# Performance work log

Measured on AMD Instinct MI355X. Metric: run time of the kernel, lower is better.

Reference implementation:

```python
import jax, jax.numpy as jnp
import numpy as np

NUM_HEADS = 16
ROPE_BASE = 10000.0


def _rope_tables(head_dim, seq_len, dtype=jnp.float32):
    # Half-split convention: rotate first half against second half.
    inv_freq = 1.0 / (ROPE_BASE ** (jnp.arange(0, head_dim, 2, dtype=dtype) / head_dim))
    pos = jnp.arange(seq_len, dtype=dtype)
    angles_half = jnp.einsum('s,d->sd', pos, inv_freq)          # (S, D/2)
    angles = jnp.concatenate([angles_half, angles_half], -1)     # (S, D)
    return jnp.cos(angles), jnp.sin(angles)


def _apply_rope(x, cos, sin):
    # x: (H, S, D); cos/sin: (S, D) broadcast over heads
    half = x.shape[-1] // 2
    x1, x2 = x[..., :half], x[..., half:]
    x_rot = jnp.concatenate([-x2, x1], axis=-1)
    return x * cos + x_rot * sin


def setup_inputs() -> dict:
    key = jax.random.key(0)
    S, E = 2048, 2048
    ks = jax.random.split(key, 9)
    sc = 0.02
    return {
        'x': jax.random.normal(ks[0], (S, E), jnp.float32),
        'Wq': jax.random.normal(ks[1], (E, E), jnp.float32) * sc,
        'bq': jax.random.normal(ks[2], (E,), jnp.float32) * sc,
        'Wk': jax.random.normal(ks[3], (E, E), jnp.float32) * sc,
        'bk': jax.random.normal(ks[4], (E,), jnp.float32) * sc,
        'Wv': jax.random.normal(ks[5], (E, E), jnp.float32) * sc,
        'bv': jax.random.normal(ks[6], (E,), jnp.float32) * sc,
        'Wo': jax.random.normal(ks[7], (E, E), jnp.float32) * sc,
        'bo': jax.random.normal(ks[8], (E,), jnp.float32) * sc,
    }


def reference(x, Wq, bq, Wk, bk, Wv, bv, Wo, bo):
    S, E = x.shape
    H = NUM_HEADS
    D = E // H
    scale = D ** 0.5
    cos, sin = _rope_tables(D, S, x.dtype)

    def proj(W, b):
        return (x @ W.T + b).reshape(S, H, D).transpose(1, 0, 2)  # (H, S, D)

    q = _apply_rope(proj(Wq, bq), cos, sin)
    k = _apply_rope(proj(Wk, bk), cos, sin)
    v = proj(Wv, bv)

    scores = jnp.einsum('hsd,htd->hst', q, k) / scale  # (H, S, S)
    attn = jax.nn.softmax(scores, axis=-1)
    out = jnp.einsum('hst,htd->hsd', attn, v)          # (H, S, D)
    # Faithful to the original's transpose(0,1).view(S,E) on a (1,H,S,D)
    # tensor: an in-order (head-major) flatten reinterpreted as (S, E).
    out = out.reshape(S, E)
    return out @ Wo.T + bo
```

## Files before the change

kernel.cpp:

```cpp
#include <hip/hip_runtime.h>

#define SDIM 2048
#define EDIM 2048
#define NHEAD 16
#define DHEAD 128

typedef __attribute__((ext_vector_type(8))) short short8;
typedef __attribute__((ext_vector_type(4))) float floatx4;

__device__ __forceinline__ float bf2f(ushort u) {
    union { uint i; float f; } v; v.i = ((uint)u) << 16; return v.f;
}
__device__ __forceinline__ ushort f2bf(float f) {
    union { float f; uint i; } v; v.f = f;
    uint r = v.i + 0x7fff + ((v.i >> 16) & 1);
    return (ushort)(r >> 16);
}

__device__ __forceinline__ void gload_lds16(const ushort* g, ushort* l) {
    __builtin_amdgcn_global_load_lds(
        (const __attribute__((address_space(1))) void*)g,
        (__attribute__((address_space(3))) void*)l, 16, 0, 0);
}

__global__ void convert5_kernel(
    const float* __restrict__ s0, const float* __restrict__ s1,
    const float* __restrict__ s2, const float* __restrict__ s3,
    const float* __restrict__ s4,
    ushort* __restrict__ d0, ushort* __restrict__ d1,
    ushort* __restrict__ d2, ushort* __restrict__ d3,
    ushort* __restrict__ d4)
{
    const float* src; ushort* dst;
    switch (blockIdx.y) {
        case 0: src = s0; dst = d0; break;
        case 1: src = s1; dst = d1; break;
        case 2: src = s2; dst = d2; break;
        case 3: src = s3; dst = d3; break;
        default: src = s4; dst = d4; break;
    }
    int i = blockIdx.x * blockDim.x + threadIdx.x;
    float4 f = ((const float4*)src)[i];
    ushort4 o;
    o.x = f2bf(f.x); o.y = f2bf(f.y); o.z = f2bf(f.z); o.w = f2bf(f.w);
    ((ushort4*)dst)[i] = o;
}

#define QPRESCALE 0.12754245f
__global__ void rope_kernel(ushort* __restrict__ Q, ushort* __restrict__ K) {
    int t = blockIdx.x * blockDim.x + threadIdx.x;
    int arr = t >> 18;
    int r = t & 0x3FFFF;
    int g = r & 7;
    int h = (r >> 3) & 15;
    int s = r >> 7;
    ushort* P = arr ? K : Q;
    float qsc = arr ? 1.0f : QPRESCALE;
    size_t base = ((size_t)s << 11) + (h << 7) + g * 8;
    union { uint4 v; ushort u[8]; } x1, x2, o1, o2;
    x1.v = *(const uint4*)(P + base);
    x2.v = *(const uint4*)(P + base + 64);
    float fs = (float)s;
#pragma unroll
    for (int j = 0; j < 8; j++) {
        int i = g * 8 + j;
        float inv = __expf((float)i * -0.14391157f);
        float ang = fs * inv;
        float rev = ang * 0.15915494309f;
        rev = rev - floorf(rev);
        float ar = rev * 6.28318530718f;
        float sn = __sinf(ar), cs = __cosf(ar);
        float a = bf2f(x1.u[j]), b = bf2f(x2.u[j]);
        o1.u[j] = f2bf((a * cs - b * sn) * qsc);
        o2.u[j] = f2bf((b * cs + a * sn) * qsc);
    }
    *(uint4*)(P + base) = o1.v;
    *(uint4*)(P + base + 64) = o2.v;
}

__device__ __forceinline__ void stout(float* p, float v)  { *p = v; }
__device__ __forceinline__ void stout(ushort* p, float v) { *p = f2bf(v); }

template <typename OUTT>
__global__ __launch_bounds__(256) void gemm_bt(
    const ushort* __restrict__ A,
    const ushort* __restrict__ B0, const ushort* __restrict__ B1, const ushort* __restrict__ B2,
    const float* __restrict__ s0, const float* __restrict__ s1, const float* __restrict__ s2,
    OUTT* __restrict__ C0, OUTT* __restrict__ C1, OUTT* __restrict__ C2,
    int nbpm, int vt_which)
{
    __shared__ __align__(16) ushort a_s[128 * 32];
    __shared__ __align__(16) ushort b_s[128 * 32];

    const int tid = threadIdx.x;
    const int wave = tid >> 6, lane = tid & 63;
    const int l15 = lane & 15, quad = lane >> 4;
    const int wm = wave & 1, wn = wave >> 1;

    const int w = blockIdx.x;
    const int xcd = w & 7, t = w >> 3;
    const int Y = gridDim.x >> 4;
    const int mtile = ((xcd & 1) << 3) | (t & 7);
    const int y = (Y >> 2) * (xcd >> 1) + (t >> 3);
    const int bm = mtile * 128;
    const int which = y / nbpm;
    const int n0 = (y % nbpm) * 128;

    const ushort* B   = (which == 0) ? B0 : (which == 1) ? B1 : B2;
    const float*  bia = (which == 0) ? s0 : (which == 1) ? s1 : s2;
    OUTT*         C   = (which == 0) ? C0 : (which == 1) ? C1 : C2;

    floatx4 acc[4][4];
#pragma unroll
    for (int i = 0; i < 4; i++)
#pragma unroll
        for (int j = 0; j < 4; j++) acc[i][j] = (floatx4)0.0f;

    const int t1 = tid + 256;
    const int row0 = tid >> 2, kc0 = (tid & 3) * 8;
    const int row1 = t1 >> 2,  kc1 = (t1 & 3) * 8;

    for (int k0 = 0; k0 < EDIM; k0 += 32) {
        __syncthreads();
        gload_lds16(A + (size_t)(bm + row0) * EDIM + k0 + kc0, a_s + tid * 8);
        gload_lds16(A + (size_t)(bm + row1) * EDIM + k0 + kc1, a_s + t1 * 8);
        gload_lds16(B + (size_t)(n0 + row0) * EDIM + k0 + kc0, b_s + tid * 8);
        gload_lds16(B + (size_t)(n0 + row1) * EDIM + k0 + kc1, b_s + t1 * 8);
        __syncthreads();

        short8 af[4], bf[4];
#pragma unroll
        for (int mt = 0; mt < 4; mt++)
            af[mt] = *(const short8*)(a_s + (wm * 64 + mt * 16 + l15) * 32 + quad * 8);
#pragma unroll
        for (int nt = 0; nt < 4; nt++)
            bf[nt] = *(const short8*)(b_s + (wn * 64 + nt * 16 + l15) * 32 + quad * 8);
#pragma unroll
        for (int mt = 0; mt < 4; mt++)
#pragma unroll
            for (int nt = 0; nt < 4; nt++)
                acc[mt][nt] = __builtin_amdgcn_mfma_f32_16x16x32_bf16(af[mt], bf[nt], acc[mt][nt], 0, 0, 0);
    }

    if (which == vt_which) {
        ushort* Cv = (ushort*)C;
#pragma unroll
        for (int nt = 0; nt < 4; nt++) {
            int col = n0 + wn * 64 + nt * 16 + l15;
            int h = col >> 7, d = col & 127;
            float bv = bia[col];
#pragma unroll
            for (int mt = 0; mt < 4; mt++) {
                int s = bm + wm * 64 + mt * 16 + quad * 4;
                ushort4 pk;
                pk.x = f2bf(acc[mt][nt][0] + bv);
                pk.y = f2bf(acc[mt][nt][1] + bv);
                pk.z = f2bf(acc[mt][nt][2] + bv);
                pk.w = f2bf(acc[mt][nt][3] + bv);
                *(ushort4*)(Cv + (size_t)h * SDIM * DHEAD + (size_t)d * SDIM + s) = pk;
            }
        }
    } else {
#pragma unroll
        for (int nt = 0; nt < 4; nt++) {
            int col = n0 + wn * 64 + nt * 16 + l15;
            float bv = bia[col];
#pragma unroll
            for (int mt = 0; mt < 4; mt++) {
#pragma unroll
                for (int r = 0; r < 4; r++) {
                    int row = bm + wm * 64 + mt * 16 + quad * 4 + r;
                    stout(&C[(size_t)row * EDIM + col], acc[mt][nt][r] + bv);
                }
            }
        }
    }
}

#define MFIX2 17.31234049f
__global__ __launch_bounds__(256, 4) void attn_kernel(
    const ushort* __restrict__ Q, const ushort* __restrict__ K,
    const ushort* __restrict__ Vtg,
    ushort* __restrict__ Opart, float* __restrict__ Lsum,
    ushort* __restrict__ Ab, int nsplit)
{
    __shared__ __align__(16) ushort Ks[64 * 128];
    __shared__ __align__(16) ushort Vt[128 * 64];
    __shared__ __align__(16) ushort Ps[64 * 64];

    const int bid = blockIdx.x;
    const int head = bid & 15, qt = (bid >> 4) & 31, half = bid >> 9;
    const int tid = threadIdx.x, wave = tid >> 6, lane = tid & 63;
    const int l15 = lane & 15, quad = lane >> 4;
    const int l7 = l15 & 7;
    const int kstart = half * (SDIM / nsplit);
    const int ntile = (SDIM / nsplit) / 64;

    short8 qf[4];
    {
        int s = qt * 64 + wave * 16 + l15;
        const ushort* qp = Q + (size_t)s * EDIM + head * DHEAD;
#pragma unroll
        for (int kc = 0; kc < 4; kc++) qf[kc] = *(const short8*)(qp + kc * 32 + quad * 8);
    }

    floatx4 o[8];
#pragma unroll
    for (int i = 0; i < 8; i++) o[i] = (floatx4)0.0f;
    float lsum = 0.0f;

    const int krow = tid >> 4, kc8 = tid & 15;
    const int vd = tid >> 3, vc8 = tid & 7;
    const int prow = wave * 16 + l15;

    for (int kv = 0; kv < ntile; kv++) {
        const int k0 = kstart + kv * 64;
        __syncthreads();
#pragma unroll
        for (int i = 0; i < 4; i++) {
            int row = krow + i * 16;
            uint4 v = *(const uint4*)(K + (size_t)(k0 + row) * EDIM + head * DHEAD + kc8 * 8);
            *(uint4*)(Ks + row * 128 + ((kc8 ^ (row & 7)) << 3)) = v;
        }
#pragma unroll
        for (int i = 0; i < 4; i++) {
            int d = vd + i * 32;
            uint4 v = *(const uint4*)(Vtg + (size_t)head * SDIM * DHEAD + (size_t)d * SDIM + k0 + vc8 * 8);
            *(uint4*)(Vt + d * 64 + ((vc8 ^ (d & 7)) << 3)) = v;
        }
        __syncthreads();

#pragma unroll
        for (int nt = 0; nt < 4; nt++) {
            floatx4 st = (floatx4)0.0f;
#pragma unroll
            for (int kc = 0; kc < 4; kc++) {
                short8 kfr = *(const short8*)(Ks + (nt * 16 + l15) * 128 + (((kc * 4 + quad) ^ l7) << 3));
                st = __builtin_amdgcn_mfma_f32_16x16x32_bf16(kfr, qf[kc], st, 0, 0, 0);
            }
            ushort4 pk;
            float p0 = __builtin_amdgcn_exp2f(st[0] - MFIX2);
            float p1 = __builtin_amdgcn_exp2f(st[1] - MFIX2);
            float p2 = __builtin_amdgcn_exp2f(st[2] - MFIX2);
            float p3 = __builtin_amdgcn_exp2f(st[3] - MFIX2);
            lsum += (p0 + p1) + (p2 + p3);
            pk.x = f2bf(p0); pk.y = f2bf(p1); pk.z = f2bf(p2); pk.w = f2bf(p3);
            int c2 = (nt * 2 + (quad >> 1)) ^ l7;
            *(ushort4*)(Ps + prow * 64 + (c2 << 3) + ((quad & 1) << 2)) = pk;
        }

#pragma unroll
        for (int kc2 = 0; kc2 < 2; kc2++) {
            short8 af = *(const short8*)(Ps + prow * 64 + (((kc2 * 4 + quad) ^ l7) << 3));
#pragma unroll
            for (int nt2 = 0; nt2 < 8; nt2++) {
                short8 bfr = *(const short8*)(Vt + (nt2 * 16 + l15) * 64 + (((kc2 * 4 + quad) ^ l7) << 3));
                o[nt2] = __builtin_amdgcn_mfma_f32_16x16x32_bf16(af, bfr, o[nt2], 0, 0, 0);
            }
        }
    }

    lsum += __shfl_xor(lsum, 16);
    lsum += __shfl_xor(lsum, 32);

    if (nsplit == 1) {
        float invl[4];
#pragma unroll
        for (int r = 0; r < 4; r++) invl[r] = 1.0f / __shfl(lsum, quad * 4 + r, 16);
#pragma unroll
        for (int nt2 = 0; nt2 < 8; nt2++) {
#pragma unroll
            for (int r = 0; r < 4; r++) {
                int s = qt * 64 + wave * 16 + quad * 4 + r;
                int d = nt2 * 16 + l15;
                Ab[(size_t)head * SDIM * DHEAD + (size_t)s * DHEAD + d] = f2bf(o[nt2][r] * invl[r]);
            }
        }
    } else {
        size_t pb = ((size_t)half * NHEAD + head) * SDIM * DHEAD;
#pragma unroll
        for (int nt2 = 0; nt2 < 8; nt2++) {
#pragma unroll
            for (int r = 0; r < 4; r++) {
                int s = qt * 64 + wave * 16 + quad * 4 + r;
                int d = nt2 * 16 + l15;
                Opart[pb + (size_t)s * DHEAD + d] = f2bf(o[nt2][r]);
            }
        }
        if (lane < 16)
            Lsum[((size_t)half * NHEAD + head) * SDIM + qt * 64 + wave * 16 + lane] = lsum;
    }
}

__global__ void merge_kernel(const ushort* __restrict__ Opart,
                             const float* __restrict__ Lsum,
                             ushort* __restrict__ Ab)
{
    int t = blockIdx.x * blockDim.x + threadIdx.x;
    int row = t >> 4, c8 = (t & 15) * 8;
    float inv = 1.0f / (Lsum[row] + Lsum[NHEAD * SDIM + row]);
    union { uint4 v; ushort u[8]; } a0, a1, ro;
    a0.v = *(const uint4*)(Opart + (size_t)row * DHEAD + c8);
    a1.v = *(const uint4*)(Opart + (size_t)(NHEAD * SDIM) * DHEAD + (size_t)row * DHEAD + c8);
#pragma unroll
    for (int j = 0; j < 8; j++)
        ro.u[j] = f2bf((bf2f(a0.u[j]) + bf2f(a1.u[j])) * inv);
    *(uint4*)(Ab + (size_t)row * DHEAD + c8) = ro.v;
}

extern "C" void kernel_launch(void* const* d_in, const int* in_sizes, int n_in,
                              void* d_out, int out_size, void* d_ws, size_t ws_size,
                              hipStream_t stream) {
    (void)in_sizes; (void)n_in; (void)out_size;
    const float* x  = (const float*)d_in[0];
    const float* Wq = (const float*)d_in[1];
    const float* bq = (const float*)d_in[2];
    const float* Wk = (const float*)d_in[3];
    const float* bk = (const float*)d_in[4];
    const float* Wv = (const float*)d_in[5];
    const float* bv = (const float*)d_in[6];
    const float* Wo = (const float*)d_in[7];
    const float* bo = (const float*)d_in[8];
    float* out = (float*)d_out;

    char* ws = (char*)d_ws;
    const size_t SEG = (size_t)EDIM * EDIM * 2;
    ushort* xb  = (ushort*)(ws + 0 * SEG);
    ushort* Wqb = (ushort*)(ws + 1 * SEG);
    ushort* Wkb = (ushort*)(ws + 2 * SEG);
    ushort* Wvb = (ushort*)(ws + 3 * SEG);
    ushort* Wob = (ushort*)(ws + 4 * SEG);
    ushort* Qb  = (ushort*)(ws + 5 * SEG);
    ushort* Kb  = (ushort*)(ws + 6 * SEG);
    ushort* Vtg = (ushort*)(ws + 7 * SEG);
    ushort* Ab  = (ushort*)(ws + 8 * SEG);
    ushort* Op  = (ushort*)(ws + 9 * SEG);
    float*  Ls  = (float*)(ws + 11 * SEG);

    const int nsplit = (ws_size >= ((size_t)89 << 20)) ? 2 : 1;

    convert5_kernel<<<dim3(4096, 5), 256, 0, stream>>>(
        x, Wq, Wk, Wv, Wo, xb, Wqb, Wkb, Wvb, Wob);

    gemm_bt<ushort><<<768, 256, 0, stream>>>(
        xb, Wqb, Wkb, Wvb, bq, bk, bv, Qb, Kb, Vtg, 16, 2);

    rope_kernel<<<2048, 256, 0, stream>>>(Qb, Kb);

    attn_kernel<<<512 * nsplit, 256, 0, stream>>>(Qb, Kb, Vtg, Op, Ls, Ab, nsplit);
    if (nsplit == 2)
        merge_kernel<<<2048, 256, 0, stream>>>(Op, Ls, Ab);

    gemm_bt<float><<<256, 256, 0, stream>>>(
        Ab, Wob, Wob, Wob, bo, bo, bo, out, out, out, 16, -1);
}
```

Baseline: 343.1 us.

## Split attention four ways and split-K the output projection GEMM

Attention work is split four ways across the key dimension instead of two, and the merge kernel now sums four partial outputs and row sums. The output projection GEMM is split along K into two halves writing fp32 partials, and a new elementwise kernel adds the partials plus the bias. The goal is more blocks for the 256-block output GEMM and the attention pass, at the cost of extra partial-buffer traffic and an extra launch. The GEMM also drops its XCD-aware block remapping for a plain 2D grid, which may hurt L2 locality.

```diff
diff --git a/kernel.cpp b/kernel.cpp
--- a/kernel.cpp
+++ b/kernel.cpp
@@ -87,7 +87,7 @@
     const ushort* __restrict__ B0, const ushort* __restrict__ B1, const ushort* __restrict__ B2,
     const float* __restrict__ s0, const float* __restrict__ s1, const float* __restrict__ s2,
     OUTT* __restrict__ C0, OUTT* __restrict__ C1, OUTT* __restrict__ C2,
-    int nbpm, int vt_which)
+    int nbpm, int vt_which, int ksplit)
 {
     __shared__ __align__(16) ushort a_s[128 * 32];
     __shared__ __align__(16) ushort b_s[128 * 32];
@@ -96,20 +96,17 @@
     const int wave = tid >> 6, lane = tid & 63;
     const int l15 = lane & 15, quad = lane >> 4;
     const int wm = wave & 1, wn = wave >> 1;
-
-    const int w = blockIdx.x;
-    const int xcd = w & 7, t = w >> 3;
-    const int Y = gridDim.x >> 4;
-    const int mtile = ((xcd & 1) << 3) | (t & 7);
-    const int y = (Y >> 2) * (xcd >> 1) + (t >> 3);
-    const int bm = mtile * 128;
-    const int which = y / nbpm;
-    const int n0 = (y % nbpm) * 128;
+    const int bm = blockIdx.x * 128;
+    const int which = blockIdx.y / nbpm;
+    const int n0 = (blockIdx.y % nbpm) * 128;
 
     const ushort* B   = (which == 0) ? B0 : (which == 1) ? B1 : B2;
     const float*  bia = (which == 0) ? s0 : (which == 1) ? s1 : s2;
     OUTT*         C   = (which == 0) ? C0 : (which == 1) ? C1 : C2;
 
+    int kbeg = 0, kend = EDIM;
+    if (ksplit == 2) { kbeg = which * (EDIM / 2); kend = kbeg + EDIM / 2; }
+
     floatx4 acc[4][4];
 #pragma unroll
     for (int i = 0; i < 4; i++)
@@ -120,7 +117,7 @@
     const int row0 = tid >> 2, kc0 = (tid & 3) * 8;
     const int row1 = t1 >> 2,  kc1 = (t1 & 3) * 8;
 
-    for (int k0 = 0; k0 < EDIM; k0 += 32) {
+    for (int k0 = kbeg; k0 < kend; k0 += 32) {
         __syncthreads();
         gload_lds16(A + (size_t)(bm + row0) * EDIM + k0 + kc0, a_s + tid * 8);
         gload_lds16(A + (size_t)(bm + row1) * EDIM + k0 + kc1, a_s + t1 * 8);
@@ -164,7 +161,7 @@
 #pragma unroll
         for (int nt = 0; nt < 4; nt++) {
             int col = n0 + wn * 64 + nt * 16 + l15;
-            float bv = bia[col];
+            float bv = bia ? bia[col] : 0.0f;
 #pragma unroll
             for (int mt = 0; mt < 4; mt++) {
 #pragma unroll
@@ -296,16 +293,35 @@
                              const float* __restrict__ Lsum,
                              ushort* __restrict__ Ab)
 {
+    const int HS = NHEAD * SDIM;
     int t = blockIdx.x * blockDim.x + threadIdx.x;
     int row = t >> 4, c8 = (t & 15) * 8;
-    float inv = 1.0f / (Lsum[row] + Lsum[NHEAD * SDIM + row]);
-    union { uint4 v; ushort u[8]; } a0, a1, ro;
-    a0.v = *(const uint4*)(Opart + (size_t)row * DHEAD + c8);
-    a1.v = *(const uint4*)(Opart + (size_t)(NHEAD * SDIM) * DHEAD + (size_t)row * DHEAD + c8);
-#pragma unroll
-    for (int j = 0; j < 8; j++)
-        ro.u[j] = f2bf((bf2f(a0.u[j]) + bf2f(a1.u[j])) * inv);
+    float inv = 1.0f / (Lsum[row] + Lsum[HS + row] + Lsum[2 * HS + row] + Lsum[3 * HS + row]);
+    float acc[8] = {0, 0, 0, 0, 0, 0, 0, 0};
+#pragma unroll
+    for (int p = 0; p < 4; p++) {
+        union { uint4 v; ushort u[8]; } a;
+        a.v = *(const uint4*)(Opart + (size_t)p * HS * DHEAD + (size_t)row * DHEAD + c8);
+#pragma unroll
+        for (int j = 0; j < 8; j++) acc[j] += bf2f(a.u[j]);
+    }
+    union { uint4 v; ushort u[8]; } ro;
+#pragma unroll
+    for (int j = 0; j < 8; j++) ro.u[j] = f2bf(acc[j] * inv);
     *(uint4*)(Ab + (size_t)row * DHEAD + c8) = ro.v;
+}
+
+__global__ void merge2_kernel(const float* __restrict__ P0, const float* __restrict__ P1,
+                              const float* __restrict__ bo, float* __restrict__ out)
+{
+    int i = blockIdx.x * blockDim.x + threadIdx.x;
+    float4 a = ((const float4*)P0)[i];
+    float4 b = ((const float4*)P1)[i];
+    float4 bb = ((const float4*)bo)[i & (EDIM / 4 - 1)];
+    float4 r;
+    r.x = a.x + b.x + bb.x; r.y = a.y + b.y + bb.y;
+    r.z = a.z + b.z + bb.z; r.w = a.w + b.w + bb.w;
+    ((float4*)out)[i] = r;
 }
 
 extern "C" void kernel_launch(void* const* d_in, const int* in_sizes, int n_in,
@@ -334,23 +350,30 @@
     ushort* Kb  = (ushort*)(ws + 6 * SEG);
     ushort* Vtg = (ushort*)(ws + 7 * SEG);
     ushort* Ab  = (ushort*)(ws + 8 * SEG);
-    ushort* Op  = (ushort*)(ws + 9 * SEG);
+    ushort* Op  = (ushort*)(ws + 0 * SEG);
+    float*  P0  = (float*)(ws + 0 * SEG);
+    float*  P1  = (float*)(ws + 2 * SEG);
     float*  Ls  = (float*)(ws + 11 * SEG);
 
-    const int nsplit = (ws_size >= ((size_t)89 << 20)) ? 2 : 1;
+    const int split = (ws_size >= ((size_t)89 << 20)) ? 1 : 0;
 
     convert5_kernel<<<dim3(4096, 5), 256, 0, stream>>>(
         x, Wq, Wk, Wv, Wo, xb, Wqb, Wkb, Wvb, Wob);
 
-    gemm_bt<ushort><<<768, 256, 0, stream>>>(
-        xb, Wqb, Wkb, Wvb, bq, bk, bv, Qb, Kb, Vtg, 16, 2);
+    gemm_bt<ushort><<<dim3(16, 48), 256, 0, stream>>>(
+        xb, Wqb, Wkb, Wvb, bq, bk, bv, Qb, Kb, Vtg, 16, 2, 1);
 
     rope_kernel<<<2048, 256, 0, stream>>>(Qb, Kb);
 
-    attn_kernel<<<512 * nsplit, 256, 0, stream>>>(Qb, Kb, Vtg, Op, Ls, Ab, nsplit);
-    if (nsplit == 2)
+    if (split) {
+        attn_kernel<<<2048, 256, 0, stream>>>(Qb, Kb, Vtg, Op, Ls, Ab, 4);
         merge_kernel<<<2048, 256, 0, stream>>>(Op, Ls, Ab);
-
-    gemm_bt<float><<<256, 256, 0, stream>>>(
-        Ab, Wob, Wob, Wob, bo, bo, bo, out, out, out, 16, -1);
-}
+        gemm_bt<float><<<dim3(16, 32), 256, 0, stream>>>(
+            Ab, Wob, Wob, Wob, nullptr, nullptr, nullptr, P0, P1, P1, 16, -1, 2);
+        merge2_kernel<<<4096, 256, 0, stream>>>(P0, P1, bo, out);
+    } else {
+        attn_kernel<<<512, 256, 0, stream>>>(Qb, Kb, Vtg, Op, Ls, Ab, 1);
+        gemm_bt<float><<<dim3(16, 16), 256, 0, stream>>>(
+            Ab, Wob, Wob, Wob, bo, bo, bo, out, out, out, 16, -1, 1);
+    }
+}
```

Result: faster. 331.0 us (-3.5%).
